# Kernel tuning notes

Measured on AMD Instinct MI355X. Metric: run time of the kernel, lower is better.

Reference implementation:

```python
import jax, jax.numpy as jnp
import numpy as np

B, N, M, S = 2, 1024, 1024, 4
D_MODEL, H = 512, 8
C = D_MODEL // H  # 64 per-head dim


def setup_inputs() -> dict:
    key = jax.random.key(0)
    ks = jax.random.split(key, 11)
    inp = {
        "input_q": jax.random.normal(ks[0], (B, N, D_MODEL), jnp.float32),
        "input_k": jax.random.normal(ks[1], (B, M, D_MODEL), jnp.float32),
        "input_v": jax.random.normal(ks[2], (B, M, D_MODEL), jnp.float32),
        "input_q_subspace": jax.random.uniform(ks[3], (B, S, N), jnp.float32),
        "input_k_subspace": jax.random.uniform(ks[4], (B, S, M), jnp.float32),
        # Linear params (torch Linear: y = x @ W.T + b)
        "Wq": jax.random.normal(ks[5], (D_MODEL, D_MODEL), jnp.float32) * 0.02,
        "bq": jnp.zeros((D_MODEL,), jnp.float32),
        "Wk": jax.random.normal(ks[6], (D_MODEL, D_MODEL), jnp.float32) * 0.02,
        "bk": jnp.zeros((D_MODEL,), jnp.float32),
        "Wv": jax.random.normal(ks[7], (D_MODEL, D_MODEL), jnp.float32) * 0.02,
        "bv": jnp.zeros((D_MODEL,), jnp.float32),
    }
    return inp


def _split_heads(x):
    # (b, n, h*c) -> (b, h, n, c)
    b, n, _ = x.shape
    return x.reshape(b, n, H, C).transpose(0, 2, 1, 3)


def reference(input_q, input_k, input_v, input_q_subspace, input_k_subspace,
              Wq, bq, Wk, bk, Wv, bv):
    q = _split_heads(input_q @ Wq.T + bq)  # (b,h,n,c)
    k = _split_heads(input_k @ Wk.T + bk)  # (b,h,m,c)
    v = _split_heads(input_v @ Wv.T + bv)  # (b,h,m,c)

    # broadcast subspace weights into a 5D tensor
    q5 = jnp.einsum('bhnc,bsn->bhsnc', q, input_q_subspace)
    k5 = jnp.einsum('bhmc,bsm->bhsmc', k, input_k_subspace)

    scale = 1.0 / np.sqrt(C).astype(np.float32)
    scores = jnp.einsum('bhsnc,bhsmc->bhsnm', q5, k5) * scale  # (b,h,s,n,m)
    attn = jax.nn.softmax(scores, axis=-1)

    hidden = jnp.einsum('bhsnm,bhmc->bhsnc', attn, v)
    # (b,h,s,n,c) -> (b,s,n,h*c)
    b, h, s, n, c = hidden.shape
    hidden = hidden.transpose(0, 2, 3, 1, 4).reshape(b, s, n, h * c)
    return hidden, attn
```

## Files before the change

### kernel.cpp

```cpp
#include <hip/hip_runtime.h>

#define BB 2
#define NN 1024
#define MM 1024
#define SS 4
#define DMODEL 512
#define HH 8
#define CC 64

typedef __attribute__((ext_vector_type(8))) short short8;
typedef __attribute__((ext_vector_type(4))) short short4v;
typedef __attribute__((ext_vector_type(4))) float f32x4;

__device__ __forceinline__ unsigned short f2bf(float x) {
    union { float f; unsigned u; } c; c.f = x;
    return (unsigned short)(c.u >> 16);
}
__device__ __forceinline__ float bf2f(unsigned short h) {
    union { float f; unsigned u; } c; c.u = ((unsigned)h) << 16;
    return c.f;
}

#define MFMA16(a, b, c) __builtin_amdgcn_mfma_f32_16x16x32_bf16(a, b, c, 0, 0, 0)

__device__ __forceinline__ void gll16(const void* g, void* l) {
    __builtin_amdgcn_global_load_lds((const __attribute__((address_space(1))) void*)g,
                                     (__attribute__((address_space(3))) void*)l, 16, 0, 0);
}

__global__ __launch_bounds__(256) void proj_kernel(
    const float* __restrict__ xq, const float* __restrict__ xk, const float* __restrict__ xv,
    const float* __restrict__ Wq, const float* __restrict__ Wk, const float* __restrict__ Wv,
    const float* __restrict__ bq, const float* __restrict__ bk, const float* __restrict__ bv,
    float* __restrict__ qout, unsigned short* __restrict__ khi,
    unsigned short* __restrict__ klo, unsigned short* __restrict__ vTg)
{
    __shared__ __align__(16) float xs[16 * 68];
    __shared__ __align__(16) float wsm[16 * 68];

    const int z = blockIdx.z;
    const float* x    = (z == 0) ? xq : (z == 1) ? xk : xv;
    const float* W    = (z == 0) ? Wq : (z == 1) ? Wk : Wv;
    const float* bias = (z == 0) ? bq : (z == 1) ? bk : bv;

    const int t   = threadIdx.x;
    const int tx  = t & 15, ty = t >> 4;
    const int r0  = blockIdx.y * 64;
    const int o0  = blockIdx.x * 64;
    const int kkq = t & 15;
    const int rr  = t >> 4;

    float4 acc[4];
    #pragma unroll
    for (int i = 0; i < 4; ++i) { acc[i].x = 0.f; acc[i].y = 0.f; acc[i].z = 0.f; acc[i].w = 0.f; }

    #pragma unroll 1
    for (int kt = 0; kt < 32; ++kt) {
        const int k0 = kt * 16;
        __syncthreads();
        #pragma unroll
        for (int i = 0; i < 4; ++i) {
            const int row = rr + i * 16;
            xs[kkq * 68 + row]  = x[(size_t)(r0 + row) * DMODEL + k0 + kkq];
            wsm[kkq * 68 + row] = W[(size_t)(o0 + row) * DMODEL + k0 + kkq];
        }
        __syncthreads();
        #pragma unroll
        for (int kk = 0; kk < 16; ++kk) {
            const float4 a  = *(const float4*)&xs[kk * 68 + ty * 4];
            const float4 w4 = *(const float4*)&wsm[kk * 68 + tx * 4];
            acc[0].x += a.x * w4.x; acc[0].y += a.x * w4.y; acc[0].z += a.x * w4.z; acc[0].w += a.x * w4.w;
            acc[1].x += a.y * w4.x; acc[1].y += a.y * w4.y; acc[1].z += a.y * w4.z; acc[1].w += a.y * w4.w;
            acc[2].x += a.z * w4.x; acc[2].y += a.z * w4.y; acc[2].z += a.z * w4.z; acc[2].w += a.z * w4.w;
            acc[3].x += a.w * w4.x; acc[3].y += a.w * w4.y; acc[3].z += a.w * w4.z; acc[3].w += a.w * w4.w;
        }
    }

    const float4 bv4 = *(const float4*)&bias[o0 + tx * 4];
    const int h = o0 >> 6;

    if (z == 0) {
        #pragma unroll
        for (int ii = 0; ii < 4; ++ii) {
            const int r = r0 + ty * 4 + ii;
            const int bb = r >> 10, n = r & 1023;
            float4 o;
            o.x = acc[ii].x + bv4.x; o.y = acc[ii].y + bv4.y;
            o.z = acc[ii].z + bv4.z; o.w = acc[ii].w + bv4.w;
            *(float4*)&qout[((size_t)(bb * HH + h) * NN + n) * CC + tx * 4] = o;
        }
    } else if (z == 1) {
        #pragma unroll
        for (int ii = 0; ii < 4; ++ii) {
            const int r = r0 + ty * 4 + ii;
            const int bb = r >> 10, m = r & 1023;
            float4 o;
            o.x = acc[ii].x + bv4.x; o.y = acc[ii].y + bv4.y;
            o.z = acc[ii].z + bv4.z; o.w = acc[ii].w + bv4.w;
            const unsigned short h0 = f2bf(o.x), h1 = f2bf(o.y), h2 = f2bf(o.z), h3 = f2bf(o.w);
            short4v hh = { (short)h0, (short)h1, (short)h2, (short)h3 };
            short4v ll = { (short)f2bf(o.x - bf2f(h0)), (short)f2bf(o.y - bf2f(h1)),
                           (short)f2bf(o.z - bf2f(h2)), (short)f2bf(o.w - bf2f(h3)) };
            const size_t base = ((size_t)(bb * HH + h) << 16) + ((size_t)m << 6)
                              + ((((tx >> 1) ^ (m & 7)) << 3) + ((tx & 1) << 2));
            *(short4v*)&khi[base] = hh;
            *(short4v*)&klo[base] = ll;
        }
    } else {
        #pragma unroll
        for (int ii = 0; ii < 4; ++ii) {
            const int r = r0 + ty * 4 + ii;
            const int bb = r >> 10, m = r & 1023;
            const size_t bhb = ((size_t)(bb * HH + h) << 16);
            const float vals[4] = { acc[ii].x + bv4.x, acc[ii].y + bv4.y,
                                    acc[ii].z + bv4.z, acc[ii].w + bv4.w };
            #pragma unroll
            for (int j = 0; j < 4; ++j) {
                const int c = tx * 4 + j;
                const size_t addr = bhb + ((size_t)c << 10) + (size_t)(m & ~63)
                                  + (((((m >> 3) & 7) ^ (c & 7)) << 3) + (m & 7));
                vTg[addr] = f2bf(vals[j]);
            }
        }
    }
}

__global__ __launch_bounds__(256, 3) void attn_kernel(
    const float* __restrict__ qws,
    const unsigned short* __restrict__ khi_g, const unsigned short* __restrict__ klo_g,
    const unsigned short* __restrict__ vT_g,
    const float* __restrict__ qsub, const float* __restrict__ ksub,
    float* __restrict__ out_hidden, float* __restrict__ out_attn)
{
    __shared__ __align__(16) unsigned char smem[50048];
    unsigned short* s_kh = (unsigned short*)smem;
    unsigned short* s_kl = s_kh + 4096;
    unsigned short* s_vT = s_kh;
    unsigned short* s_at = s_kh + 4096;
    float* s_S  = (float*)(smem + 16384);
    unsigned short* s_qh = (unsigned short*)(smem + 16384);
    unsigned short* s_ql = s_qh + 16 * 72;
    float* s_qs  = (float*)(smem + 49280);
    float* s_inv = (float*)(smem + 49408);

    const int t     = threadIdx.x;
    const int blk   = blockIdx.x;
    const int ntile = blk & 127;
    const int bh    = blk >> 7;
    const int b     = bh >> 3;
    const int h     = bh & 7;
    const int n0    = ntile * 8;

    const int lane = t & 63;
    const int w    = t >> 6;
    const int l15  = lane & 15;
    const int quad = lane >> 4;

    if (t < 128) {
        const int row = t >> 4, c4 = t & 15;
        const float4 qv = *(const float4*)&qws[((size_t)bh * NN + n0 + row) * CC + c4 * 4];
        const unsigned short h0 = f2bf(qv.x), h1 = f2bf(qv.y), h2 = f2bf(qv.z), h3 = f2bf(qv.w);
        short4v hh = { (short)h0, (short)h1, (short)h2, (short)h3 };
        short4v ll = { (short)f2bf(qv.x - bf2f(h0)), (short)f2bf(qv.y - bf2f(h1)),
                       (short)f2bf(qv.z - bf2f(h2)), (short)f2bf(qv.w - bf2f(h3)) };
        *(short4v*)&s_qh[row * 72 + c4 * 4] = hh;
        *(short4v*)&s_ql[row * 72 + c4 * 4] = ll;
    }
    for (int i = 576 + t; i < 1152; i += 256) { s_qh[i] = 0; s_ql[i] = 0; }
    if (t < 32) s_qs[t] = qsub[((size_t)b * SS + (t >> 3)) * NN + n0 + (t & 7)] * 0.125f;
    __syncthreads();

    const short8 qh0 = *(const short8*)&s_qh[l15 * 72 + 0  + quad * 8];
    const short8 qh1 = *(const short8*)&s_qh[l15 * 72 + 32 + quad * 8];
    const short8 ql0 = *(const short8*)&s_ql[l15 * 72 + 0  + quad * 8];
    const short8 ql1 = *(const short8*)&s_ql[l15 * 72 + 32 + quad * 8];

    const unsigned short* kh_g = khi_g + ((size_t)bh << 16);
    const unsigned short* kl_g = klo_g + ((size_t)bh << 16);

    #pragma unroll 1
    for (int mt = 0; mt < 16; ++mt) {
        const int m0 = mt << 6;
        #pragma unroll
        for (int i = 0; i < 4; ++i) {
            const int idx = w * 4 + i;
            const int j   = ((idx & 7) << 6) + lane;
            const unsigned short* src = ((idx < 8) ? kh_g : kl_g)
                                      + ((size_t)(m0 + (j >> 3)) << 6) + ((j & 7) << 3);
            gll16(src, s_kh + (idx << 9));
        }
        __syncthreads();

        const int krow = (w << 4) + l15;
        const int sw   = krow & 7;
        const short8 kh0f = *(const short8*)&s_kh[(krow << 6) + ((quad ^ sw) << 3)];
        const short8 kh1f = *(const short8*)&s_kh[(krow << 6) + (((4 | quad) ^ sw) << 3)];
        const short8 kl0f = *(const short8*)&s_kl[(krow << 6) + ((quad ^ sw) << 3)];
        const short8 kl1f = *(const short8*)&s_kl[(krow << 6) + (((4 | quad) ^ sw) << 3)];
        f32x4 acc = {0.f, 0.f, 0.f, 0.f};
        acc = MFMA16(qh0, kh0f, acc);
        acc = MFMA16(qh1, kh1f, acc);
        acc = MFMA16(ql0, kh0f, acc);
        acc = MFMA16(ql1, kh1f, acc);
        acc = MFMA16(qh0, kl0f, acc);
        acc = MFMA16(qh1, kl1f, acc);

        if (quad < 2) {
            const int mglob = m0 + krow;
            #pragma unroll
            for (int r = 0; r < 4; ++r)
                s_S[(quad * 4 + r) * 1028 + mglob] = acc[r];
        }
        __syncthreads();
    }

    const unsigned short* vg = vT_g + ((size_t)bh << 16);
    auto stage_v = [&](int m0v) {
        #pragma unroll
        for (int i = 0; i < 2; ++i) {
            const int idx = (w << 1) + i;
            const int j   = (idx << 6) + lane;
            const unsigned short* src = vg + ((size_t)(j >> 3) << 10) + m0v + ((j & 7) << 3);
            gll16(src, s_vT + (idx << 9));
        }
    };
    stage_v(0);

    {
        const int sn = t >> 3, mg = t & 7;
        const int sD = sn >> 3, nD = sn & 7;
        const float qsD = s_qs[sn];
        const float* ksD  = ksub + ((size_t)b * SS + sD) * MM + (mg << 7);
        const float* Srow = s_S + nD * 1028 + (mg << 7);
        float d = 0.f;
        #pragma unroll 4
        for (int ii = 0; ii < 32; ++ii) {
            const int i = (ii + mg) & 31;
            const f32x4  Sv = *(const f32x4*)&Srow[i << 2];
            const float4 kv = *(const float4*)&ksD[i << 2];
            d += __expf(Sv[0] * qsD * kv.x) + __expf(Sv[1] * qsD * kv.y)
               + __expf(Sv[2] * qsD * kv.z) + __expf(Sv[3] * qsD * kv.w);
        }
        d += __shfl_xor(d, 1); d += __shfl_xor(d, 2); d += __shfl_xor(d, 4);
        if (mg == 0) s_inv[sn] = 1.0f / d;
    }
    __syncthreads();

    const int sn = t >> 3, mg = t & 7;
    const int sC = sn >> 3, nC = sn & 7;
    const float invC = s_inv[sn];
    const float qsC  = s_qs[sn];
    const float* ksC = ksub + ((size_t)b * SS + sC) * MM;
    float* attnC = out_attn + (((size_t)(bh * SS + sC)) * NN + n0 + nC) * MM;
    const int Mt = w >> 1, nsel = w & 1;
    f32x4 av0 = {0.f, 0.f, 0.f, 0.f}, av1 = {0.f, 0.f, 0.f, 0.f};

    #pragma unroll 1
    for (int mt = 0; mt < 16; ++mt) {
        const int m0 = mt << 6;
        {
            const f32x4 S0 = *(const f32x4*)&s_S[nC * 1028 + m0 + (mg << 3)];
            const f32x4 S1 = *(const f32x4*)&s_S[nC * 1028 + m0 + (mg << 3) + 4];
            const float4 k0 = *(const float4*)&ksC[m0 + (mg << 3)];
            const float4 k1 = *(const float4*)&ksC[m0 + (mg << 3) + 4];
            float4 e0, e1;
            e0.x = __expf(S0[0] * qsC * k0.x) * invC;
            e0.y = __expf(S0[1] * qsC * k0.y) * invC;
            e0.z = __expf(S0[2] * qsC * k0.z) * invC;
            e0.w = __expf(S0[3] * qsC * k0.w) * invC;
            e1.x = __expf(S1[0] * qsC * k1.x) * invC;
            e1.y = __expf(S1[1] * qsC * k1.y) * invC;
            e1.z = __expf(S1[2] * qsC * k1.z) * invC;
            e1.w = __expf(S1[3] * qsC * k1.w) * invC;
            *(float4*)&attnC[m0 + (mg << 3)]     = e0;
            *(float4*)&attnC[m0 + (mg << 3) + 4] = e1;
            short8 pk = { (short)f2bf(e0.x), (short)f2bf(e0.y), (short)f2bf(e0.z), (short)f2bf(e0.w),
                          (short)f2bf(e1.x), (short)f2bf(e1.y), (short)f2bf(e1.z), (short)f2bf(e1.w) };
            *(short8*)&s_at[sn * 72 + (mg << 3)] = pk;
        }
        asm volatile("s_waitcnt vmcnt(2) lgkmcnt(0)" ::: "memory");
        __builtin_amdgcn_sched_barrier(0);
        __builtin_amdgcn_s_barrier();
        __builtin_amdgcn_sched_barrier(0);

        #pragma unroll
        for (int Ks = 0; Ks < 2; ++Ks) {
            const int c0r = (nsel << 4) + l15, c1r = ((nsel + 2) << 4) + l15;
            const int swv = l15 & 7;
            const short8 a   = *(const short8*)&s_at[((Mt << 4) + l15) * 72 + (Ks << 5) + (quad << 3)];
            const short8 vb0 = *(const short8*)&s_vT[(c0r << 6) + ((((Ks << 2) | quad) ^ swv) << 3)];
            const short8 vb1 = *(const short8*)&s_vT[(c1r << 6) + ((((Ks << 2) | quad) ^ swv) << 3)];
            av0 = MFMA16(a, vb0, av0);
            av1 = MFMA16(a, vb1, av1);
        }
        asm volatile("s_waitcnt lgkmcnt(0)" ::: "memory");
        __builtin_amdgcn_sched_barrier(0);
        __builtin_amdgcn_s_barrier();
        __builtin_amdgcn_sched_barrier(0);
        if (mt < 15) stage_v(m0 + 64);
        __builtin_amdgcn_sched_barrier(0);
    }

    #pragma unroll
    for (int r = 0; r < 4; ++r) {
        const int snr = Mt * 16 + quad * 4 + r;
        const int s = snr >> 3, n = snr & 7;
        float* orow = out_hidden + (((size_t)b * SS + s) * NN + n0 + n) * DMODEL + h * CC;
        orow[nsel * 16 + l15]       = av0[r];
        orow[(nsel + 2) * 16 + l15] = av1[r];
    }
}

extern "C" void kernel_launch(void* const* d_in, const int* in_sizes, int n_in,
                              void* d_out, int out_size, void* d_ws, size_t ws_size,
                              hipStream_t stream) {
    const float* xq   = (const float*)d_in[0];
    const float* xk   = (const float*)d_in[1];
    const float* xv   = (const float*)d_in[2];
    const float* qsub = (const float*)d_in[3];
    const float* ksub = (const float*)d_in[4];
    const float* Wq   = (const float*)d_in[5];
    const float* bq   = (const float*)d_in[6];
    const float* Wk   = (const float*)d_in[7];
    const float* bk   = (const float*)d_in[8];
    const float* Wv   = (const float*)d_in[9];
    const float* bv   = (const float*)d_in[10];

    float* ws = (float*)d_ws;
    float* qf = ws;
    unsigned short* khi = (unsigned short*)(ws + 1048576);
    unsigned short* klo = khi + 1048576;
    unsigned short* vTg = klo + 1048576;

    float* out_hidden = (float*)d_out;
    float* out_attn   = out_hidden + (size_t)BB * SS * NN * DMODEL;

    proj_kernel<<<dim3(8, 32, 3), 256, 0, stream>>>(xq, xk, xv, Wq, Wk, Wv, bq, bk, bv,
                                                    qf, khi, klo, vTg);
    attn_kernel<<<dim3(2048), 256, 0, stream>>>(qf, khi, klo, vTg,
                                                qsub, ksub, out_hidden, out_attn);
}
```

Before: 408.8 us.

## Move projection GEMM to split-bf16 MFMA and fold softmax normalization into exp2

The projection kernel's scalar FP32 FMA loop is replaced by MFMA 16x16x32 bf16 instructions using a hi/lo split (three products) to keep near-FP32 accuracy. Inputs go through swizzled LDS tiles with 64-wide K steps. The V transpose is now staged through LDS so the global stores are coalesced. In the attention kernel, exp is changed to exp2 with log2(e) folded into the q scale, and the reciprocal multiply is replaced by adding -log2(sum) inside the exponent. The split-bf16 scheme adds conversion work and small accuracy risk, and the log-domain normalization relies on the hardware exp2/log approximations.

```diff
diff --git a/kernel.cpp b/kernel.cpp
--- a/kernel.cpp
+++ b/kernel.cpp
@@ -20,6 +20,7 @@
     union { float f; unsigned u; } c; c.u = ((unsigned)h) << 16;
     return c.f;
 }
+__device__ __forceinline__ float fexp2(float x) { return __builtin_amdgcn_exp2f(x); }
 
 #define MFMA16(a, b, c) __builtin_amdgcn_mfma_f32_16x16x32_bf16(a, b, c, 0, 0, 0)
 
@@ -35,93 +36,133 @@
     float* __restrict__ qout, unsigned short* __restrict__ khi,
     unsigned short* __restrict__ klo, unsigned short* __restrict__ vTg)
 {
-    __shared__ __align__(16) float xs[16 * 68];
-    __shared__ __align__(16) float wsm[16 * 68];
+    __shared__ __align__(16) unsigned short s_xh[64 * 64];
+    __shared__ __align__(16) unsigned short s_xl[64 * 64];
+    __shared__ __align__(16) unsigned short s_wh[64 * 64];
+    __shared__ __align__(16) unsigned short s_wl[64 * 64];
 
     const int z = blockIdx.z;
     const float* x    = (z == 0) ? xq : (z == 1) ? xk : xv;
     const float* W    = (z == 0) ? Wq : (z == 1) ? Wk : Wv;
     const float* bias = (z == 0) ? bq : (z == 1) ? bk : bv;
 
-    const int t   = threadIdx.x;
-    const int tx  = t & 15, ty = t >> 4;
-    const int r0  = blockIdx.y * 64;
-    const int o0  = blockIdx.x * 64;
-    const int kkq = t & 15;
-    const int rr  = t >> 4;
-
-    float4 acc[4];
+    const int t    = threadIdx.x;
+    const int lane = t & 63;
+    const int w    = t >> 6;
+    const int l15  = lane & 15;
+    const int quad = lane >> 4;
+    const int r0   = blockIdx.y * 64;
+    const int o0   = blockIdx.x * 64;
+
+    f32x4 acc[4];
     #pragma unroll
-    for (int i = 0; i < 4; ++i) { acc[i].x = 0.f; acc[i].y = 0.f; acc[i].z = 0.f; acc[i].w = 0.f; }
+    for (int i = 0; i < 4; ++i) acc[i] = (f32x4){0.f, 0.f, 0.f, 0.f};
+
+    const int srow = t >> 4, sc4 = t & 15;
 
     #pragma unroll 1
-    for (int kt = 0; kt < 32; ++kt) {
-        const int k0 = kt * 16;
+    for (int kt = 0; kt < 8; ++kt) {
+        const int k0 = kt * 64;
         __syncthreads();
         #pragma unroll
         for (int i = 0; i < 4; ++i) {
-            const int row = rr + i * 16;
-            xs[kkq * 68 + row]  = x[(size_t)(r0 + row) * DMODEL + k0 + kkq];
-            wsm[kkq * 68 + row] = W[(size_t)(o0 + row) * DMODEL + k0 + kkq];
-        }
-        __syncthreads();
-        #pragma unroll
-        for (int kk = 0; kk < 16; ++kk) {
-            const float4 a  = *(const float4*)&xs[kk * 68 + ty * 4];
-            const float4 w4 = *(const float4*)&wsm[kk * 68 + tx * 4];
-            acc[0].x += a.x * w4.x; acc[0].y += a.x * w4.y; acc[0].z += a.x * w4.z; acc[0].w += a.x * w4.w;
-            acc[1].x += a.y * w4.x; acc[1].y += a.y * w4.y; acc[1].z += a.y * w4.z; acc[1].w += a.y * w4.w;
-            acc[2].x += a.z * w4.x; acc[2].y += a.z * w4.y; acc[2].z += a.z * w4.z; acc[2].w += a.z * w4.w;
-            acc[3].x += a.w * w4.x; acc[3].y += a.w * w4.y; acc[3].z += a.w * w4.z; acc[3].w += a.w * w4.w;
-        }
-    }
-
-    const float4 bv4 = *(const float4*)&bias[o0 + tx * 4];
+            const int row = srow + i * 16;
+            const int pos = (row << 6) + ((((sc4 >> 1) ^ (row & 7)) << 3) + ((sc4 & 1) << 2));
+            {
+                const float4 v = *(const float4*)&x[(size_t)(r0 + row) * DMODEL + k0 + sc4 * 4];
+                const unsigned short h0 = f2bf(v.x), h1 = f2bf(v.y), h2 = f2bf(v.z), h3 = f2bf(v.w);
+                short4v hh = { (short)h0, (short)h1, (short)h2, (short)h3 };
+                short4v ll = { (short)f2bf(v.x - bf2f(h0)), (short)f2bf(v.y - bf2f(h1)),
+                               (short)f2bf(v.z - bf2f(h2)), (short)f2bf(v.w - bf2f(h3)) };
+                *(short4v*)&s_xh[pos] = hh;
+                *(short4v*)&s_xl[pos] = ll;
+            }
+            {
+                const float4 v = *(const float4*)&W[(size_t)(o0 + row) * DMODEL + k0 + sc4 * 4];
+                const unsigned short h0 = f2bf(v.x), h1 = f2bf(v.y), h2 = f2bf(v.z), h3 = f2bf(v.w);
+                short4v hh = { (short)h0, (short)h1, (short)h2, (short)h3 };
+                short4v ll = { (short)f2bf(v.x - bf2f(h0)), (short)f2bf(v.y - bf2f(h1)),
+                               (short)f2bf(v.z - bf2f(h2)), (short)f2bf(v.w - bf2f(h3)) };
+                *(short4v*)&s_wh[pos] = hh;
+                *(short4v*)&s_wl[pos] = ll;
+            }
+        }
+        __syncthreads();
+
+        const int arow = (w << 4) + l15;
+        const int asw  = arow & 7;
+        const short8 ah0 = *(const short8*)&s_xh[(arow << 6) + ((quad ^ asw) << 3)];
+        const short8 ah1 = *(const short8*)&s_xh[(arow << 6) + (((4 | quad) ^ asw) << 3)];
+        const short8 al0 = *(const short8*)&s_xl[(arow << 6) + ((quad ^ asw) << 3)];
+        const short8 al1 = *(const short8*)&s_xl[(arow << 6) + (((4 | quad) ^ asw) << 3)];
+        #pragma unroll
+        for (int ct = 0; ct < 4; ++ct) {
+            const int brow = (ct << 4) + l15;
+            const int bsw  = brow & 7;
+            const short8 bh0 = *(const short8*)&s_wh[(brow << 6) + ((quad ^ bsw) << 3)];
+            const short8 bh1 = *(const short8*)&s_wh[(brow << 6) + (((4 | quad) ^ bsw) << 3)];
+            const short8 bl0 = *(const short8*)&s_wl[(brow << 6) + ((quad ^ bsw) << 3)];
+            const short8 bl1 = *(const short8*)&s_wl[(brow << 6) + (((4 | quad) ^ bsw) << 3)];
+            acc[ct] = MFMA16(ah0, bh0, acc[ct]);
+            acc[ct] = MFMA16(ah1, bh1, acc[ct]);
+            acc[ct] = MFMA16(al0, bh0, acc[ct]);
+            acc[ct] = MFMA16(al1, bh1, acc[ct]);
+            acc[ct] = MFMA16(ah0, bl0, acc[ct]);
+            acc[ct] = MFMA16(ah1, bl1, acc[ct]);
+        }
+    }
+
     const int h = o0 >> 6;
-
     if (z == 0) {
         #pragma unroll
-        for (int ii = 0; ii < 4; ++ii) {
-            const int r = r0 + ty * 4 + ii;
-            const int bb = r >> 10, n = r & 1023;
-            float4 o;
-            o.x = acc[ii].x + bv4.x; o.y = acc[ii].y + bv4.y;
-            o.z = acc[ii].z + bv4.z; o.w = acc[ii].w + bv4.w;
-            *(float4*)&qout[((size_t)(bb * HH + h) * NN + n) * CC + tx * 4] = o;
+        for (int r = 0; r < 4; ++r) {
+            const int rg = r0 + (w << 4) + (quad << 2) + r;
+            const int bb = rg >> 10, n = rg & 1023;
+            float* orow = qout + ((size_t)(bb * HH + h) * NN + n) * CC;
+            #pragma unroll
+            for (int ct = 0; ct < 4; ++ct)
+                orow[(ct << 4) + l15] = acc[ct][r] + bias[o0 + (ct << 4) + l15];
         }
     } else if (z == 1) {
         #pragma unroll
-        for (int ii = 0; ii < 4; ++ii) {
-            const int r = r0 + ty * 4 + ii;
-            const int bb = r >> 10, m = r & 1023;
-            float4 o;
-            o.x = acc[ii].x + bv4.x; o.y = acc[ii].y + bv4.y;
-            o.z = acc[ii].z + bv4.z; o.w = acc[ii].w + bv4.w;
-            const unsigned short h0 = f2bf(o.x), h1 = f2bf(o.y), h2 = f2bf(o.z), h3 = f2bf(o.w);
-            short4v hh = { (short)h0, (short)h1, (short)h2, (short)h3 };
-            short4v ll = { (short)f2bf(o.x - bf2f(h0)), (short)f2bf(o.y - bf2f(h1)),
-                           (short)f2bf(o.z - bf2f(h2)), (short)f2bf(o.w - bf2f(h3)) };
-            const size_t base = ((size_t)(bb * HH + h) << 16) + ((size_t)m << 6)
-                              + ((((tx >> 1) ^ (m & 7)) << 3) + ((tx & 1) << 2));
-            *(short4v*)&khi[base] = hh;
-            *(short4v*)&klo[base] = ll;
+        for (int r = 0; r < 4; ++r) {
+            const int rg = r0 + (w << 4) + (quad << 2) + r;
+            const int bb = rg >> 10, m = rg & 1023;
+            const size_t base = ((size_t)(bb * HH + h) << 16) + ((size_t)m << 6);
+            const int msw = m & 7;
+            #pragma unroll
+            for (int ct = 0; ct < 4; ++ct) {
+                const int c = (ct << 4) + l15;
+                const float o = acc[ct][r] + bias[o0 + c];
+                const unsigned short hh = f2bf(o);
+                const unsigned short ll = f2bf(o - bf2f(hh));
+                const size_t addr = base + ((((c >> 3) ^ msw) << 3) + (c & 7));
+                khi[addr] = hh;
+                klo[addr] = ll;
+            }
         }
     } else {
-        #pragma unroll
-        for (int ii = 0; ii < 4; ++ii) {
-            const int r = r0 + ty * 4 + ii;
-            const int bb = r >> 10, m = r & 1023;
-            const size_t bhb = ((size_t)(bb * HH + h) << 16);
-            const float vals[4] = { acc[ii].x + bv4.x, acc[ii].y + bv4.y,
-                                    acc[ii].z + bv4.z, acc[ii].w + bv4.w };
+        __syncthreads();
+        unsigned short* s_t = s_xh;
+        #pragma unroll
+        for (int r = 0; r < 4; ++r) {
+            const int m_l = (w << 4) + (quad << 2) + r;
             #pragma unroll
-            for (int j = 0; j < 4; ++j) {
-                const int c = tx * 4 + j;
-                const size_t addr = bhb + ((size_t)c << 10) + (size_t)(m & ~63)
-                                  + (((((m >> 3) & 7) ^ (c & 7)) << 3) + (m & 7));
-                vTg[addr] = f2bf(vals[j]);
+            for (int ct = 0; ct < 4; ++ct) {
+                const int c = (ct << 4) + l15;
+                const float o = acc[ct][r] + bias[o0 + c];
+                s_t[(c << 6) + ((((m_l >> 3) ^ (c & 7)) << 3) + (m_l & 7))] = f2bf(o);
             }
         }
+        __syncthreads();
+        const int bb = r0 >> 10, m0 = r0 & 1023;
+        const size_t bhb = ((size_t)(bb * HH + h) << 16);
+        const int c = t >> 2, part = t & 3;
+        const short8 v0 = *(const short8*)&s_t[(c << 6) + (part << 4)];
+        const short8 v1 = *(const short8*)&s_t[(c << 6) + (part << 4) + 8];
+        unsigned short* dst = vTg + bhb + ((size_t)c << 10) + m0 + (part << 4);
+        *(short8*)&dst[0] = v0;
+        *(short8*)&dst[8] = v1;
     }
 }
 
@@ -167,7 +208,8 @@
         *(short4v*)&s_ql[row * 72 + c4 * 4] = ll;
     }
     for (int i = 576 + t; i < 1152; i += 256) { s_qh[i] = 0; s_ql[i] = 0; }
-    if (t < 32) s_qs[t] = qsub[((size_t)b * SS + (t >> 3)) * NN + n0 + (t & 7)] * 0.125f;
+    if (t < 32) s_qs[t] = qsub[((size_t)b * SS + (t >> 3)) * NN + n0 + (t & 7)]
+                        * (0.125f * 1.44269504088896f);
     __syncthreads();
 
     const short8 qh0 = *(const short8*)&s_qh[l15 * 72 + 0  + quad * 8];
@@ -238,18 +280,18 @@
             const int i = (ii + mg) & 31;
             const f32x4  Sv = *(const f32x4*)&Srow[i << 2];
             const float4 kv = *(const float4*)&ksD[i << 2];
-            d += __expf(Sv[0] * qsD * kv.x) + __expf(Sv[1] * qsD * kv.y)
-               + __expf(Sv[2] * qsD * kv.z) + __expf(Sv[3] * qsD * kv.w);
+            d += fexp2(Sv[0] * qsD * kv.x) + fexp2(Sv[1] * qsD * kv.y)
+               + fexp2(Sv[2] * qsD * kv.z) + fexp2(Sv[3] * qsD * kv.w);
         }
         d += __shfl_xor(d, 1); d += __shfl_xor(d, 2); d += __shfl_xor(d, 4);
-        if (mg == 0) s_inv[sn] = 1.0f / d;
+        if (mg == 0) s_inv[sn] = -__builtin_amdgcn_logf(d);
     }
     __syncthreads();
 
     const int sn = t >> 3, mg = t & 7;
     const int sC = sn >> 3, nC = sn & 7;
-    const float invC = s_inv[sn];
-    const float qsC  = s_qs[sn];
+    const float linvC = s_inv[sn];
+    const float qsC   = s_qs[sn];
     const float* ksC = ksub + ((size_t)b * SS + sC) * MM;
     float* attnC = out_attn + (((size_t)(bh * SS + sC)) * NN + n0 + nC) * MM;
     const int Mt = w >> 1, nsel = w & 1;
@@ -264,14 +306,14 @@
             const float4 k0 = *(const float4*)&ksC[m0 + (mg << 3)];
             const float4 k1 = *(const float4*)&ksC[m0 + (mg << 3) + 4];
             float4 e0, e1;
-            e0.x = __expf(S0[0] * qsC * k0.x) * invC;
-            e0.y = __expf(S0[1] * qsC * k0.y) * invC;
-            e0.z = __expf(S0[2] * qsC * k0.z) * invC;
-            e0.w = __expf(S0[3] * qsC * k0.w) * invC;
-            e1.x = __expf(S1[0] * qsC * k1.x) * invC;
-            e1.y = __expf(S1[1] * qsC * k1.y) * invC;
-            e1.z = __expf(S1[2] * qsC * k1.z) * invC;
-            e1.w = __expf(S1[3] * qsC * k1.w) * invC;
+            e0.x = fexp2(fmaf(S0[0] * qsC, k0.x, linvC));
+            e0.y = fexp2(fmaf(S0[1] * qsC, k0.y, linvC));
+            e0.z = fexp2(fmaf(S0[2] * qsC, k0.z, linvC));
+            e0.w = fexp2(fmaf(S0[3] * qsC, k0.w, linvC));
+            e1.x = fexp2(fmaf(S1[0] * qsC, k1.x, linvC));
+            e1.y = fexp2(fmaf(S1[1] * qsC, k1.y, linvC));
+            e1.z = fexp2(fmaf(S1[2] * qsC, k1.z, linvC));
+            e1.w = fexp2(fmaf(S1[3] * qsC, k1.w, linvC));
             *(float4*)&attnC[m0 + (mg << 3)]     = e0;
             *(float4*)&attnC[m0 + (mg << 3) + 4] = e1;
             short8 pk = { (short)f2bf(e0.x), (short)f2bf(e0.y), (short)f2bf(e0.z), (short)f2bf(e0.w),
```

Result: faster. 376.5 us (-7.9%).
